# Performance work log

Hardware: AMD Instinct MI355X
Metric: run time of the kernel (lower is better)

Reference implementation:

```python
import jax, jax.numpy as jnp
import numpy as np

PATCH = 300
B, F = 16, 14
NOISE_FACTOR = 0.1
KERNEL = 7  # MedianPool2d(7, same=True) -> reflect pad 3 each side
PAD = 3
MED_IDX = (KERNEL * KERNEL - 1) // 2  # lower median of 49 = index 24


def median_pool7(x):
    """x: [C,H,W] -> [C,H,W], 7x7 median with reflect 'same' padding (MedianPool2d)."""
    C, H, W = x.shape
    xp = jnp.pad(x, ((0, 0), (PAD, PAD), (PAD, PAD)), mode='reflect')
    # 49 shifted views stacked on last axis: [C,H,W,49]
    wins = jnp.stack([xp[:, i:i + H, j:j + W]
                      for i in range(KERNEL) for j in range(KERNEL)], axis=-1)
    return jnp.sort(wins, axis=-1)[..., MED_IDX]


def setup_inputs() -> dict:
    key = jax.random.key(0)
    k1, k2, k3, k4, k5 = jax.random.split(key, 5)
    adv_patch = jax.random.uniform(k1, (3, PATCH, PATCH), dtype=jnp.float32)
    lab_batch = jax.random.uniform(k2, (B, F, 5), dtype=jnp.float32)
    contrast = jax.random.uniform(k3, (B, F), dtype=jnp.float32, minval=0.8, maxval=1.2)
    brightness = jax.random.uniform(k4, (B, F), dtype=jnp.float32, minval=-0.1, maxval=0.1)
    noise = jax.random.uniform(k5, (B, F, 3, PATCH, PATCH), dtype=jnp.float32, minval=-1.0, maxval=1.0)
    return {"adv_patch": adv_patch, "lab_batch": lab_batch, "contrast": contrast,
            "brightness": brightness, "noise": noise, "img_size": 416}


def reference(adv_patch, lab_batch, contrast, brightness, noise, img_size):
    # adv_patch side (300) <= img_size (416): interpolation branch skipped.
    p = median_pool7(adv_patch)                      # enable_blurred=True
    b, f = lab_batch.shape[0], lab_batch.shape[1]
    adv_batch = jnp.broadcast_to(p[None, None], (b, f) + p.shape)  # [B,F,3,P,P]
    c = contrast[:, :, None, None, None]
    br = brightness[:, :, None, None, None]
    adv_batch = adv_batch * c + br + noise * NOISE_FACTOR
    # with_black_trans=False branch
    return jnp.clip(adv_batch, 1e-6, 0.99999)
```

## Files before the change

kernel.cpp:

```cpp
#include <hip/hip_runtime.h>

#define PATCH    300
#define CHW      (PATCH*PATCH)
#define NPATCH   (3*CHW)
#define NSLAB    (16*14)
#define NF4      (NPATCH/4)

#define PMED_OFF 0

static __device__ __forceinline__ float bf2f(unsigned int bits16) {
    return __uint_as_float(bits16 << 16);
}

static __device__ __forceinline__ int detect_f32(const void* patchv) {
    const uint4* p4 = (const uint4*)patchv;
    uint4 v = p4[threadIdx.x & 63];
    return __any(((v.x | v.y | v.z | v.w) & 0x80008000u) != 0u);
}

#define CSWAP(x, y) do { float t_ = fminf(x, y); (y) = fmaxf(x, y); (x) = t_; } while (0)

template <bool F32>
static __device__ __forceinline__ float ldv(const void* pc, int off) {
    return F32 ? ((const float*)pc)[off]
               : bf2f(((const unsigned short*)pc)[off]);
}

template <bool F32>
static __device__ __forceinline__ float median49(const void* pc,
                                                 const int* ro, const int* ww) {
    float a[26];
#pragma unroll
    for (int k = 0; k < 26; ++k)
        a[k] = ldv<F32>(pc, ro[k / 7] + ww[k % 7]);

    float nxt = ldv<F32>(pc, ro[26 / 7] + ww[26 % 7]);
#pragma unroll
    for (int it = 0; it < 23; ++it) {
#pragma unroll
        for (int i = it + 1; i <= 25; ++i) CSWAP(a[it], a[i]);
#pragma unroll
        for (int i = it + 1; i < 25; ++i)  CSWAP(a[i], a[25]);
        a[25] = nxt;
        if (it < 22) {
            const int k = 27 + it;
            nxt = ldv<F32>(pc, ro[k / 7] + ww[k % 7]);
        }
    }
    float mn = fminf(a[23], a[24]);
    float mx = fmaxf(a[23], a[24]);
    return fmaxf(mn, fminf(mx, a[25]));
}

__global__ __launch_bounds__(256) void median7_kernel(
        const void* __restrict__ patchv,
        float* __restrict__ pmed) {
    int mode = detect_f32(patchv);
    int idx = blockIdx.x * 256 + threadIdx.x;
    if (idx >= NPATCH) return;
    int c   = idx / CHW;
    int rem = idx - c * CHW;
    int h   = rem / PATCH;
    int w   = rem - h * PATCH;

    int ro[7], ww[7];
#pragma unroll
    for (int d = 0; d < 7; d++) {
        int x = h + d - 3;
        x = x < 0 ? -x : (x >= PATCH ? 2 * PATCH - 2 - x : x);
        ro[d] = x * PATCH;
        int y = w + d - 3;
        ww[d] = y < 0 ? -y : (y >= PATCH ? 2 * PATCH - 2 - y : y);
    }

    float med;
    if (mode) {
        med = median49<true >((const void*)((const float*)patchv + c * CHW), ro, ww);
    } else {
        med = median49<false>((const void*)((const unsigned short*)patchv + c * CHW), ro, ww);
    }
    pmed[idx] = med;
}

#define CLIP1(p, n) fminf(fmaxf((p) * c + br + (n) * 0.1f, 1e-6f), 0.99999f)

__global__ __launch_bounds__(256) void apply_kernel(
        const float* __restrict__ pmed,
        const void* __restrict__ patchv,
        const void* __restrict__ noisev,
        const void* __restrict__ contrastv,
        const void* __restrict__ brightnessv,
        float* __restrict__ out) {
    int mode = detect_f32(patchv);
    int slab = blockIdx.y;
    int j0   = blockIdx.x * 1024 + threadIdx.x;
    size_t s4 = (size_t)slab * NF4;
    const float4* pm4 = (const float4*)pmed;
    float4*       o4  = (float4*)out + s4;

    float c, br;
    if (mode) {
        c  = ((const float*)contrastv)[slab];
        br = ((const float*)brightnessv)[slab];
    } else {
        c  = bf2f(((const unsigned short*)contrastv)[slab]);
        br = bf2f(((const unsigned short*)brightnessv)[slab]);
    }

    bool full = (j0 + 3 * 256) < NF4;

    if (mode) {
        const float4* n4 = (const float4*)noisev + s4;
        if (full) {
            float4 p[4], n[4];
#pragma unroll
            for (int k = 0; k < 4; ++k) p[k] = pm4[j0 + k * 256];
#pragma unroll
            for (int k = 0; k < 4; ++k) n[k] = n4[j0 + k * 256];
#pragma unroll
            for (int k = 0; k < 4; ++k) {
                float4 r;
                r.x = CLIP1(p[k].x, n[k].x);
                r.y = CLIP1(p[k].y, n[k].y);
                r.z = CLIP1(p[k].z, n[k].z);
                r.w = CLIP1(p[k].w, n[k].w);
                o4[j0 + k * 256] = r;
            }
        } else {
#pragma unroll
            for (int k = 0; k < 4; ++k) {
                int j = j0 + k * 256;
                if (j < NF4) {
                    float4 p = pm4[j], n = n4[j];
                    float4 r;
                    r.x = CLIP1(p.x, n.x);
                    r.y = CLIP1(p.y, n.y);
                    r.z = CLIP1(p.z, n.z);
                    r.w = CLIP1(p.w, n.w);
                    o4[j] = r;
                }
            }
        }
    } else {
        const uint2* n2 = (const uint2*)noisev + s4;
        if (full) {
            float4 p[4];
            uint2  nv[4];
#pragma unroll
            for (int k = 0; k < 4; ++k) p[k]  = pm4[j0 + k * 256];
#pragma unroll
            for (int k = 0; k < 4; ++k) nv[k] = n2[j0 + k * 256];
#pragma unroll
            for (int k = 0; k < 4; ++k) {
                float4 r;
                r.x = CLIP1(p[k].x, bf2f(nv[k].x & 0xffffu));
                r.y = CLIP1(p[k].y, bf2f(nv[k].x >> 16));
                r.z = CLIP1(p[k].z, bf2f(nv[k].y & 0xffffu));
                r.w = CLIP1(p[k].w, bf2f(nv[k].y >> 16));
                o4[j0 + k * 256] = r;
            }
        } else {
#pragma unroll
            for (int k = 0; k < 4; ++k) {
                int j = j0 + k * 256;
                if (j < NF4) {
                    float4 p  = pm4[j];
                    uint2  nv = n2[j];
                    float4 r;
                    r.x = CLIP1(p.x, bf2f(nv.x & 0xffffu));
                    r.y = CLIP1(p.y, bf2f(nv.x >> 16));
                    r.z = CLIP1(p.z, bf2f(nv.y & 0xffffu));
                    r.w = CLIP1(p.w, bf2f(nv.y >> 16));
                    o4[j] = r;
                }
            }
        }
    }
}

extern "C" void kernel_launch(void* const* d_in, const int* in_sizes, int n_in,
                              void* d_out, int out_size, void* d_ws, size_t ws_size,
                              hipStream_t stream) {
    const void* adv_patch  = d_in[0];
    const void* contrast   = d_in[2];
    const void* brightness = d_in[3];
    const void* noise      = d_in[4];

    float* pmed = (float*)((char*)d_ws + PMED_OFF);
    float* out  = (float*)d_out;

    median7_kernel<<<dim3((NPATCH + 255) / 256), dim3(256), 0, stream>>>(
        adv_patch, pmed);

    dim3 g2((NF4 + 1023) / 1024, NSLAB);
    apply_kernel<<<g2, dim3(256), 0, stream>>>(
        pmed, adv_patch, noise, contrast, brightness, out);
}
```

Measured before the change: 417.0 us.

## Compute four medians per thread from a register tile and widen apply to 8 elements

The median kernel now has each thread load a 7x10 window into registers once and compute four adjacent outputs from it. This cuts redundant global loads and writes results as 16-byte vectors, at the cost of more registers and a quarter as many threads. The apply kernel handles 8 elements per thread with nontemporal loads and stores for noise and output, aiming at wider memory transactions and less cache pollution on the streaming data. The apply kernel moves roughly 200MB and dominates the runtime, so memory-path efficiency is the main lever.

```diff
diff --git a/kernel.cpp b/kernel.cpp
--- a/kernel.cpp
+++ b/kernel.cpp
@@ -4,9 +4,15 @@
 #define CHW      (PATCH*PATCH)
 #define NPATCH   (3*CHW)
 #define NSLAB    (16*14)
-#define NF4      (NPATCH/4)
+#define G8       (NPATCH/8)
+#define NQ       (NPATCH/4)
+#define QROW     (PATCH/4)
+#define QCHW     (CHW/4)
 
 #define PMED_OFF 0
+
+typedef float        f32x4 __attribute__((ext_vector_type(4)));
+typedef unsigned int u32x4 __attribute__((ext_vector_type(4)));
 
 static __device__ __forceinline__ float bf2f(unsigned int bits16) {
     return __uint_as_float(bits16 << 16);
@@ -20,21 +26,12 @@
 
 #define CSWAP(x, y) do { float t_ = fminf(x, y); (y) = fmaxf(x, y); (x) = t_; } while (0)
 
-template <bool F32>
-static __device__ __forceinline__ float ldv(const void* pc, int off) {
-    return F32 ? ((const float*)pc)[off]
-               : bf2f(((const unsigned short*)pc)[off]);
-}
-
-template <bool F32>
-static __device__ __forceinline__ float median49(const void* pc,
-                                                 const int* ro, const int* ww) {
+template <int K>
+static __device__ __forceinline__ float median49_tile(const float (&t)[7][10]) {
     float a[26];
 #pragma unroll
-    for (int k = 0; k < 26; ++k)
-        a[k] = ldv<F32>(pc, ro[k / 7] + ww[k % 7]);
-
-    float nxt = ldv<F32>(pc, ro[26 / 7] + ww[26 % 7]);
+    for (int m = 0; m < 26; ++m) a[m] = t[m / 7][K + m % 7];
+    float nxt = t[26 / 7][K + 26 % 7];
 #pragma unroll
     for (int it = 0; it < 23; ++it) {
 #pragma unroll
@@ -43,8 +40,8 @@
         for (int i = it + 1; i < 25; ++i)  CSWAP(a[i], a[25]);
         a[25] = nxt;
         if (it < 22) {
-            const int k = 27 + it;
-            nxt = ldv<F32>(pc, ro[k / 7] + ww[k % 7]);
+            const int m = 27 + it;
+            nxt = t[m / 7][K + m % 7];
         }
     }
     float mn = fminf(a[23], a[24]);
@@ -52,34 +49,51 @@
     return fmaxf(mn, fminf(mx, a[25]));
 }
 
+template <bool F32>
+static __device__ __forceinline__ void load_tile(const void* pc, const int* ro,
+                                                 const int* cc, float (&t)[7][10]) {
+#pragma unroll
+    for (int i = 0; i < 7; ++i)
+#pragma unroll
+        for (int j = 0; j < 10; ++j)
+            t[i][j] = F32 ? ((const float*)pc)[ro[i] + cc[j]]
+                          : bf2f(((const unsigned short*)pc)[ro[i] + cc[j]]);
+}
+
 __global__ __launch_bounds__(256) void median7_kernel(
         const void* __restrict__ patchv,
         float* __restrict__ pmed) {
     int mode = detect_f32(patchv);
-    int idx = blockIdx.x * 256 + threadIdx.x;
-    if (idx >= NPATCH) return;
-    int c   = idx / CHW;
-    int rem = idx - c * CHW;
-    int h   = rem / PATCH;
-    int w   = rem - h * PATCH;
+    int q = blockIdx.x * 256 + threadIdx.x;
+    if (q >= NQ) return;
+    int c   = q / QCHW;
+    int rem = q - c * QCHW;
+    int h   = rem / QROW;
+    int w0  = (rem - h * QROW) * 4;
 
-    int ro[7], ww[7];
+    int ro[7], cc[10];
 #pragma unroll
-    for (int d = 0; d < 7; d++) {
+    for (int d = 0; d < 7; ++d) {
         int x = h + d - 3;
         x = x < 0 ? -x : (x >= PATCH ? 2 * PATCH - 2 - x : x);
         ro[d] = x * PATCH;
-        int y = w + d - 3;
-        ww[d] = y < 0 ? -y : (y >= PATCH ? 2 * PATCH - 2 - y : y);
+    }
+#pragma unroll
+    for (int d = 0; d < 10; ++d) {
+        int y = w0 + d - 3;
+        cc[d] = y < 0 ? -y : (y >= PATCH ? 2 * PATCH - 2 - y : y);
     }
 
-    float med;
-    if (mode) {
-        med = median49<true >((const void*)((const float*)patchv + c * CHW), ro, ww);
-    } else {
-        med = median49<false>((const void*)((const unsigned short*)patchv + c * CHW), ro, ww);
-    }
-    pmed[idx] = med;
+    float t[7][10];
+    if (mode) load_tile<true >((const void*)((const float*)patchv + c * CHW), ro, cc, t);
+    else      load_tile<false>((const void*)((const unsigned short*)patchv + c * CHW), ro, cc, t);
+
+    f32x4 r;
+    r[0] = median49_tile<0>(t);
+    r[1] = median49_tile<1>(t);
+    r[2] = median49_tile<2>(t);
+    r[3] = median49_tile<3>(t);
+    ((f32x4*)pmed)[q] = r;
 }
 
 #define CLIP1(p, n) fminf(fmaxf((p) * c + br + (n) * 0.1f, 1e-6f), 0.99999f)
@@ -94,9 +108,6 @@
     int mode = detect_f32(patchv);
     int slab = blockIdx.y;
     int j0   = blockIdx.x * 1024 + threadIdx.x;
-    size_t s4 = (size_t)slab * NF4;
-    const float4* pm4 = (const float4*)pmed;
-    float4*       o4  = (float4*)out + s4;
 
     float c, br;
     if (mode) {
@@ -107,72 +118,48 @@
         br = bf2f(((const unsigned short*)brightnessv)[slab]);
     }
 
-    bool full = (j0 + 3 * 256) < NF4;
+    const f32x4* pm4 = (const f32x4*)pmed;
+    f32x4*       o4  = (f32x4*)out + (size_t)slab * (2 * G8);
+    bool full = (j0 + 3 * 256) < G8;
 
     if (mode) {
-        const float4* n4 = (const float4*)noisev + s4;
-        if (full) {
-            float4 p[4], n[4];
+        const f32x4* n4 = (const f32x4*)noisev + (size_t)slab * (2 * G8);
 #pragma unroll
-            for (int k = 0; k < 4; ++k) p[k] = pm4[j0 + k * 256];
+        for (int k = 0; k < 4; ++k) {
+            int j = j0 + k * 256;
+            if (full || j < G8) {
+                f32x4 pa = pm4[2 * j], pb = pm4[2 * j + 1];
+                f32x4 na = __builtin_nontemporal_load(&n4[2 * j]);
+                f32x4 nb = __builtin_nontemporal_load(&n4[2 * j + 1]);
+                f32x4 ra, rb;
 #pragma unroll
-            for (int k = 0; k < 4; ++k) n[k] = n4[j0 + k * 256];
-#pragma unroll
-            for (int k = 0; k < 4; ++k) {
-                float4 r;
-                r.x = CLIP1(p[k].x, n[k].x);
-                r.y = CLIP1(p[k].y, n[k].y);
-                r.z = CLIP1(p[k].z, n[k].z);
-                r.w = CLIP1(p[k].w, n[k].w);
-                o4[j0 + k * 256] = r;
-            }
-        } else {
-#pragma unroll
-            for (int k = 0; k < 4; ++k) {
-                int j = j0 + k * 256;
-                if (j < NF4) {
-                    float4 p = pm4[j], n = n4[j];
-                    float4 r;
-                    r.x = CLIP1(p.x, n.x);
-                    r.y = CLIP1(p.y, n.y);
-                    r.z = CLIP1(p.z, n.z);
-                    r.w = CLIP1(p.w, n.w);
-                    o4[j] = r;
+                for (int i = 0; i < 4; ++i) {
+                    ra[i] = CLIP1(pa[i], na[i]);
+                    rb[i] = CLIP1(pb[i], nb[i]);
                 }
+                __builtin_nontemporal_store(ra, &o4[2 * j]);
+                __builtin_nontemporal_store(rb, &o4[2 * j + 1]);
             }
         }
     } else {
-        const uint2* n2 = (const uint2*)noisev + s4;
-        if (full) {
-            float4 p[4];
-            uint2  nv[4];
+        const u32x4* n4 = (const u32x4*)noisev + (size_t)slab * G8;
 #pragma unroll
-            for (int k = 0; k < 4; ++k) p[k]  = pm4[j0 + k * 256];
-#pragma unroll
-            for (int k = 0; k < 4; ++k) nv[k] = n2[j0 + k * 256];
-#pragma unroll
-            for (int k = 0; k < 4; ++k) {
-                float4 r;
-                r.x = CLIP1(p[k].x, bf2f(nv[k].x & 0xffffu));
-                r.y = CLIP1(p[k].y, bf2f(nv[k].x >> 16));
-                r.z = CLIP1(p[k].z, bf2f(nv[k].y & 0xffffu));
-                r.w = CLIP1(p[k].w, bf2f(nv[k].y >> 16));
-                o4[j0 + k * 256] = r;
-            }
-        } else {
-#pragma unroll
-            for (int k = 0; k < 4; ++k) {
-                int j = j0 + k * 256;
-                if (j < NF4) {
-                    float4 p  = pm4[j];
-                    uint2  nv = n2[j];
-                    float4 r;
-                    r.x = CLIP1(p.x, bf2f(nv.x & 0xffffu));
-                    r.y = CLIP1(p.y, bf2f(nv.x >> 16));
-                    r.z = CLIP1(p.z, bf2f(nv.y & 0xffffu));
-                    r.w = CLIP1(p.w, bf2f(nv.y >> 16));
-                    o4[j] = r;
-                }
+        for (int k = 0; k < 4; ++k) {
+            int j = j0 + k * 256;
+            if (full || j < G8) {
+                f32x4 pa = pm4[2 * j], pb = pm4[2 * j + 1];
+                u32x4 nv = __builtin_nontemporal_load(&n4[j]);
+                f32x4 ra, rb;
+                ra[0] = CLIP1(pa[0], bf2f(nv[0] & 0xffffu));
+                ra[1] = CLIP1(pa[1], bf2f(nv[0] >> 16));
+                ra[2] = CLIP1(pa[2], bf2f(nv[1] & 0xffffu));
+                ra[3] = CLIP1(pa[3], bf2f(nv[1] >> 16));
+                rb[0] = CLIP1(pb[0], bf2f(nv[2] & 0xffffu));
+                rb[1] = CLIP1(pb[1], bf2f(nv[2] >> 16));
+                rb[2] = CLIP1(pb[2], bf2f(nv[3] & 0xffffu));
+                rb[3] = CLIP1(pb[3], bf2f(nv[3] >> 16));
+                __builtin_nontemporal_store(ra, &o4[2 * j]);
+                __builtin_nontemporal_store(rb, &o4[2 * j + 1]);
             }
         }
     }
@@ -189,10 +176,10 @@
     float* pmed = (float*)((char*)d_ws + PMED_OFF);
     float* out  = (float*)d_out;
 
-    median7_kernel<<<dim3((NPATCH + 255) / 256), dim3(256), 0, stream>>>(
+    median7_kernel<<<dim3((NQ + 255) / 256), dim3(256), 0, stream>>>(
         adv_patch, pmed);
 
-    dim3 g2((NF4 + 1023) / 1024, NSLAB);
+    dim3 g2((G8 + 1023) / 1024, NSLAB);
     apply_kernel<<<g2, dim3(256), 0, stream>>>(
         pmed, adv_patch, noise, contrast, brightness, out);
 }
```

Result: slower. 454.7 us (+9.0%).
